# Performance work log

Hardware: AMD Instinct MI355X
Metric: run time of the kernel (lower is better)

The kernel has to match this reference:

```python
import jax, jax.numpy as jnp
import numpy as np


def _prelu(x, a):
    return jnp.where(x >= 0, x, a * x)


def setup_inputs() -> dict:
    key = jax.random.key(0)
    ks = jax.random.split(key, 10)
    B, N, h_dim, H_dim, g_dim, Kc, n = 64, 4096, 256, 1024, 512, 32, 2048
    hs = jax.random.normal(ks[0], (B, N, h_dim), dtype=jnp.float32)
    cs_o = jax.random.randint(ks[1], (B, N), 0, Kc, dtype=jnp.int32)

    def lin(k, fi, fo):
        return jax.random.normal(k, (fi, fo), dtype=jnp.float32) / np.sqrt(fi).astype(np.float32)

    a = jnp.full((1,), 0.25, dtype=jnp.float32)  # torch PReLU default
    return {
        "hs": hs,
        "W1": lin(ks[2], h_dim, H_dim), "b1": jnp.zeros((H_dim,), jnp.float32), "a1": a,
        "W2": lin(ks[3], H_dim, H_dim), "b2": jnp.zeros((H_dim,), jnp.float32), "a2": a,
        "W3": lin(ks[4], H_dim, H_dim), "b3": jnp.zeros((H_dim,), jnp.float32), "a3": a,
        "W4": lin(ks[5], H_dim, H_dim), "b4": jnp.zeros((H_dim,), jnp.float32), "a4": a,
        "W5": lin(ks[6], H_dim, H_dim), "b5": jnp.zeros((H_dim,), jnp.float32), "a5": a,
        "W6": lin(ks[7], H_dim, g_dim), "b6": jnp.zeros((g_dim,), jnp.float32),
        "cs_o": cs_o,
        "n": n,
    }


def reference(hs, W1, b1, a1, W2, b2, a2, W3, b3, a3, W4, b4, a4, W5, b5, a5, W6, b6, cs_o, n):
    B, N, h_dim = hs.shape
    cs = cs_o.at[:, n:].set(-1)                  # points >= n are unassigned
    K = int(jnp.max(cs)) + 1                      # static (concrete data)
    Ks = jnp.max(cs, axis=1)                      # [B] max cluster id per batch entry

    # per-cluster masked sums (vectorized segment-sum over all K at once)
    onehot = (cs[:, :, None] == jnp.arange(K)[None, None, :]).astype(hs.dtype)  # [B,N,K]
    Hk = jnp.einsum('bnk,bnh->bkh', onehot, hs)   # [B,K,h] sum of hs per cluster
    hn = hs[:, n, :]                              # [B,h] the point being assigned
    # H = [H_0..H_{K-1}, H_0+h_n..H_{K-1}+h_n, h_n]
    H = jnp.concatenate([Hk, Hk + hn[:, None, :], hn[:, None, :]], axis=1)  # [B,2K+1,h]

    mk = (jnp.sum(onehot, axis=1) > 0).astype(hs.dtype)  # [B,K] cluster non-empty
    gs_mask = jnp.concatenate([mk, mk, jnp.ones((B, 1), hs.dtype)], axis=1)[:, :, None]

    # 6-layer MLP g applied to all B*(2K+1) rows at once
    x = H.reshape(B * (2 * K + 1), h_dim)
    x = _prelu(x @ W1 + b1, a1)
    x = _prelu(x @ W2 + b2, a2)
    x = _prelu(x @ W3 + b3, a3)
    x = _prelu(x @ W4 + b4, a4)
    x = _prelu(x @ W5 + b5, a5)
    gs = (x @ W6 + b6).reshape(B, 2 * K + 1, -1) * gs_mask  # [B,2K+1,g]

    # G_k = sum_{j<K, j!=k} gs_j + gs_{k+K} ;  G_K = sum_{j<K} gs_j + gs_{2K}
    S = jnp.sum(gs[:, :K], axis=1)                                   # [B,g]
    G_head = (S[:, None, :] - gs[:, :K] + gs[:, K:2 * K]) * mk[:, :, None]
    G_last = S + gs[:, 2 * K]
    G = jnp.concatenate([G_head, G_last[:, None, :]], axis=1)        # [B,K+1,g]

    # per-batch correction: if Ks[b]==k (k<K-1), move G[b,-1] to slot k+1, zero last
    need = (Ks >= 0) & (Ks < K - 1)
    kidx = jnp.arange(K + 1)
    move = need[:, None] & (kidx[None, :] == (Ks + 1)[:, None])      # [B,K+1]
    G = jnp.where(move[:, :, None], G[:, K:K + 1, :], G)
    G = jnp.where((need[:, None] & (kidx[None, :] == K))[:, :, None], 0.0, G)
    G_mask = jnp.where(need[:, None] & (kidx[None, :] >= (Ks + 2)[:, None]),
                       0.0, jnp.ones((B, K + 1), hs.dtype))
    return (G, G_mask)
```

## Files before the change

### kernel.cpp

```cpp
#include <hip/hip_runtime.h>
#include <hip/hip_bf16.h>
#include <stdint.h>

using bf16x8 = __attribute__((ext_vector_type(8))) short;
using f32x4  = __attribute__((ext_vector_type(4))) float;

#define BATCH 64
#define NTOK  4096
#define HD    256
#define HDIM  1024
#define GD    512

__device__ __forceinline__ ushort f2bf(float f) {
  union { __hip_bfloat16 h; ushort u; } cv;
  cv.h = __float2bfloat16(f);
  return cv.u;
}

__device__ __forceinline__ void gload_lds16(const void* gsrc, void* ldst) {
  typedef const __attribute__((address_space(1))) uint32_t* gas_p;
  typedef __attribute__((address_space(3))) uint32_t* las_p;
  __builtin_amdgcn_global_load_lds((gas_p)(uintptr_t)gsrc, (las_p)(uintptr_t)ldst, 16, 0, 0);
}

struct WTArgs {
  const float* src[6];
  ushort* dst[6];
  int fi[6];
  int fo[6];
};

__global__ __launch_bounds__(256) void pre_kernel(WTArgs a,
                                                  const int* __restrict__ cs,
                                                  const int* __restrict__ nptr,
                                                  int* __restrict__ idx,
                                                  int* __restrict__ off,
                                                  int* __restrict__ cnt,
                                                  int* __restrict__ Ks,
                                                  int K) {
  __shared__ int csb[NTOK];
  __shared__ int hist[256 * 32];
  __shared__ int btot[32];
  __shared__ int bbase[32];
  __shared__ float tile[32][33];
  int t = threadIdx.x;
  if (blockIdx.x < BATCH) {
    int b = blockIdx.x;
    int n = *nptr;
    const int* csrow = cs + (size_t)b * NTOK;
    int mymax = -1;
    for (int i = t; i < n; i += 256) { int v = csrow[i]; csb[i] = v; mymax = max(mymax, v); }
#pragma unroll
    for (int k = 0; k < 32; ++k) hist[t * 32 + k] = 0;
    __syncthreads();
    int chunkN = (n + 255) >> 8;
    for (int c = 0; c < chunkN; ++c) {
      int i = c * 256 + t;
      if (i < n) hist[t * 32 + csb[i]]++;
    }
    __syncthreads();
    if (t < K) {
      int run = 0;
      for (int r = 0; r < 256; ++r) { int tmp = hist[r * 32 + t]; hist[r * 32 + t] = run; run += tmp; }
      btot[t] = run;
    }
    __syncthreads();
    if (t == 0) {
      int base = 0;
      for (int k = 0; k < K; ++k) { bbase[k] = base; base += btot[k]; }
    }
    __syncthreads();
    if (t < K) { off[b * K + t] = bbase[t]; cnt[b * K + t] = btot[t]; }
    int* idxb = idx + (size_t)b * NTOK;
    for (int c = 0; c < chunkN; ++c) {
      int i = c * 256 + t;
      if (i < n) {
        int k = csb[i];
        int s = bbase[k] + hist[t * 32 + k]++;
        idxb[s] = i;
      }
    }
    for (int o2 = 32; o2; o2 >>= 1) mymax = max(mymax, __shfl_down(mymax, o2));
    if ((t & 63) == 0) btot[16 + (t >> 6)] = mymax;
    __syncthreads();
    if (t == 0) {
      int r = btot[16];
      for (int i = 1; i < 4; ++i) r = max(r, btot[16 + i]);
      Ks[b] = r;
    }
  } else {
    int f = blockIdx.x - BATCH;
    int z = 0;
    while (true) {
      int nb = (a.fo[z] >> 5) * (a.fi[z] >> 5);
      if (f < nb) break;
      f -= nb; ++z;
    }
    int ncx = a.fo[z] >> 5;
    int cx = f % ncx, cy = f / ncx;
    int c0 = cx * 32, r0 = cy * 32;
    int fo = a.fo[z], fi = a.fi[z];
    const float* W = a.src[z];
    ushort* Wt = a.dst[z];
    int tx = t & 31, ty = t >> 5;
#pragma unroll
    for (int j = 0; j < 4; ++j)
      tile[ty + j * 8][tx] = W[(size_t)(r0 + ty + j * 8) * fo + (c0 + tx)];
    __syncthreads();
#pragma unroll
    for (int j = 0; j < 4; ++j)
      Wt[(size_t)(c0 + ty + j * 8) * fi + (r0 + tx)] = f2bf(tile[tx][ty + j * 8]);
  }
}

__global__ __launch_bounds__(256) void aggregate2_kernel(const float* __restrict__ hs,
                                                         const int* __restrict__ idx,
                                                         const int* __restrict__ off,
                                                         const int* __restrict__ cnt,
                                                         const int* __restrict__ nptr,
                                                         ushort* __restrict__ X,
                                                         int K, int M, int Mpad) {
  int b = blockIdx.x / K, k = blockIdx.x % K;
  int t = threadIdx.x;
  int g = t >> 6, l = t & 63;
  int n = *nptr;
  int c = cnt[b * K + k];
  int o = off[b * K + k];
  const float* hsb = hs + (size_t)b * NTOK * HD;
  const int* ids = idx + (size_t)b * NTOK + o;
  __shared__ int sid[256];
  __shared__ float part[4][HD];
  float ax = 0.f, ay = 0.f, az = 0.f, aw = 0.f;
  float bx = 0.f, by = 0.f, bz = 0.f, bw = 0.f;
  for (int j0 = 0; j0 < c; j0 += 256) {
    __syncthreads();
    if (j0 + t < c) sid[t] = ids[j0 + t];
    __syncthreads();
    int lim = min(256, c - j0);
    int j = g;
    for (; j + 4 < lim; j += 8) {
      float4 v0 = ((const float4*)&hsb[(size_t)sid[j] * HD])[l];
      float4 v1 = ((const float4*)&hsb[(size_t)sid[j + 4] * HD])[l];
      ax += v0.x; ay += v0.y; az += v0.z; aw += v0.w;
      bx += v1.x; by += v1.y; bz += v1.z; bw += v1.w;
    }
    for (; j < lim; j += 4) {
      float4 v = ((const float4*)&hsb[(size_t)sid[j] * HD])[l];
      ax += v.x; ay += v.y; az += v.z; aw += v.w;
    }
  }
  part[g][l * 4 + 0] = ax + bx;
  part[g][l * 4 + 1] = ay + by;
  part[g][l * 4 + 2] = az + bz;
  part[g][l * 4 + 3] = aw + bw;
  __syncthreads();
  float sum = ((part[0][t] + part[1][t]) + (part[2][t] + part[3][t]));
  float hn = hsb[(size_t)n * HD + t];
  int R = 2 * K + 1;
  X[((size_t)b * R + k) * HD + t]     = f2bf(sum);
  X[((size_t)b * R + K + k) * HD + t] = f2bf(sum + hn);
  if (k == 0) {
    X[((size_t)b * R + 2 * K) * HD + t] = f2bf(hn);
    for (int r = M + b; r < Mpad; r += BATCH) X[(size_t)r * HD + t] = 0;
  }
}

template <bool LAST>
__global__ __launch_bounds__(256) void gemm_kernel(const ushort* __restrict__ A,
                                                   const ushort* __restrict__ Bt,
                                                   const float* __restrict__ bias,
                                                   const float* __restrict__ aptr,
                                                   void* __restrict__ Cout,
                                                   int N, int Kd) {
  __shared__ ushort As[3][2][128 * 32];
  __shared__ ushort Bs[3][2][64 * 32];
  int tid = threadIdx.x;
  int lane = tid & 63, w = tid >> 6;
  int wr = w >> 1, wc = w & 1;
  int fr = lane & 15, fq = lane >> 4;

  int nwg = gridDim.x;
  int flat = blockIdx.x;
  int q8 = nwg >> 3, r8 = nwg & 7;
  int xcd = flat & 7, loc = flat >> 3;
  int swz = (xcd < r8 ? xcd * (q8 + 1) : r8 * (q8 + 1) + (xcd - r8) * q8) + loc;
  int NC = N >> 6;
  int brow = swz / NC, bcol = swz % NC;

  size_t row0 = (size_t)brow * 128;
  size_t col0 = (size_t)bcol * 64;

  const ushort* Abase = A + row0 * (size_t)Kd;
  const ushort* Bbase = Bt + col0 * (size_t)Kd;

  f32x4 acc[4][2] = {};

  int qA0 = w * 64 + lane;
  int qA1 = 256 + w * 64 + lane;
  int rA0 = qA0 >> 2, kA0 = (qA0 & 3) * 8;
  int rA1 = qA1 >> 2, kA1 = (qA1 & 3) * 8;
  int rB = qA0 >> 2, kB = (qA0 & 3) * 8;

  auto stage = [&](int buf, int k0) {
#pragma unroll
    for (int h = 0; h < 2; ++h) {
      int kh = k0 + h * 32;
      gload_lds16(Abase + (size_t)rA0 * Kd + kh + kA0, &As[buf][h][(w)     * 512]);
      gload_lds16(Abase + (size_t)rA1 * Kd + kh + kA1, &As[buf][h][(4 + w) * 512]);
      gload_lds16(Bbase + (size_t)rB  * Kd + kh + kB,  &Bs[buf][h][(w)     * 512]);
    }
  };

  int nt = Kd >> 6;
  stage(0, 0);
  stage(1, 64);
  for (int t = 0; t < nt; ++t) {
    if (t + 1 < nt) asm volatile("s_waitcnt vmcnt(6)" ::: "memory");
    else            asm volatile("s_waitcnt vmcnt(0)" ::: "memory");
    __builtin_amdgcn_s_barrier();
    __builtin_amdgcn_sched_barrier(0);
    int cur = t % 3;
    bf16x8 af[2][4], bfv[2][2];
#pragma unroll
    for (int h = 0; h < 2; ++h) {
#pragma unroll
      for (int m = 0; m < 4; ++m)
        af[h][m] = *(const bf16x8*)&As[cur][h][(wr * 64 + m * 16 + fr) * 32 + fq * 8];
#pragma unroll
      for (int nn = 0; nn < 2; ++nn)
        bfv[h][nn] = *(const bf16x8*)&Bs[cur][h][(wc * 32 + nn * 16 + fr) * 32 + fq * 8];
    }
    __builtin_amdgcn_s_setprio(1);
#pragma unroll
    for (int h = 0; h < 2; ++h)
#pragma unroll
      for (int m = 0; m < 4; ++m)
#pragma unroll
        for (int nn = 0; nn < 2; ++nn)
          acc[m][nn] = __builtin_amdgcn_mfma_f32_16x16x32_bf16(af[h][m], bfv[h][nn], acc[m][nn], 0, 0, 0);
    __builtin_amdgcn_s_setprio(0);
    if (t + 2 < nt) stage((t + 2) % 3, (t + 2) * 64);
  }

  float alpha = 0.f;
  if (!LAST) alpha = aptr[0];
#pragma unroll
  for (int nn = 0; nn < 2; ++nn) {
    size_t col = col0 + wc * 32 + nn * 16 + fr;
    float bv = bias[col];
#pragma unroll
    for (int m = 0; m < 4; ++m) {
      size_t rbase = row0 + wr * 64 + m * 16 + fq * 4;
#pragma unroll
      for (int j = 0; j < 4; ++j) {
        float v = acc[m][nn][j] + bv;
        if (!LAST) {
          v = (v >= 0.f) ? v : alpha * v;
          ((ushort*)Cout)[(rbase + j) * N + col] = f2bf(v);
        } else {
          ((float*)Cout)[(rbase + j) * N + col] = v;
        }
      }
    }
  }
}

__global__ __launch_bounds__(256) void final_kernel(const float* __restrict__ gs,
                                                    const int* __restrict__ counts,
                                                    const int* __restrict__ Ks,
                                                    float* __restrict__ out,
                                                    int K) {
  int b = blockIdx.x, t = threadIdx.x;
  __shared__ float mk[64];
  __shared__ int sks;
  if (t < K) mk[t] = (counts[b * K + t] > 0) ? 1.f : 0.f;
  if (t == 0) sks = Ks[b];
  __syncthreads();
  int ks = sks;
  bool need = (ks >= 0) && (ks < K - 1);
  const float* g = gs + (size_t)b * (2 * K + 1) * GD;
  float S0 = 0.f, S1 = 0.f;
  for (int k = 0; k < K; ++k) {
    S0 += g[(size_t)k * GD + t] * mk[k];
    S1 += g[(size_t)k * GD + t + 256] * mk[k];
  }
  float gl0 = S0 + g[(size_t)(2 * K) * GD + t];
  float gl1 = S1 + g[(size_t)(2 * K) * GD + t + 256];
  float* G  = out + (size_t)b * (K + 1) * GD;
  float* Gm = out + (size_t)BATCH * (K + 1) * GD + (size_t)b * (K + 1);
  for (int kk = 0; kk <= K; ++kk) {
    float v0, v1;
    if (kk == K)                  { v0 = need ? 0.f : gl0; v1 = need ? 0.f : gl1; }
    else if (need && kk == ks + 1){ v0 = gl0;              v1 = gl1; }
    else {
      v0 = mk[kk] * (S0 - g[(size_t)kk * GD + t]       + g[(size_t)(K + kk) * GD + t]);
      v1 = mk[kk] * (S1 - g[(size_t)kk * GD + t + 256] + g[(size_t)(K + kk) * GD + t + 256]);
    }
    G[(size_t)kk * GD + t]       = v0;
    G[(size_t)kk * GD + t + 256] = v1;
  }
  if (t <= K) Gm[t] = (need && t >= ks + 2) ? 0.f : 1.f;
}

extern "C" void kernel_launch(void* const* d_in, const int* in_sizes, int n_in,
                              void* d_out, int out_size, void* d_ws, size_t ws_size,
                              hipStream_t stream) {
  const float* hs = (const float*)d_in[0];
  const float* W[6]  = {(const float*)d_in[1], (const float*)d_in[4], (const float*)d_in[7],
                        (const float*)d_in[10], (const float*)d_in[13], (const float*)d_in[16]};
  const float* bb[6] = {(const float*)d_in[2], (const float*)d_in[5], (const float*)d_in[8],
                        (const float*)d_in[11], (const float*)d_in[14], (const float*)d_in[17]};
  const float* aa[5] = {(const float*)d_in[3], (const float*)d_in[6], (const float*)d_in[9],
                        (const float*)d_in[12], (const float*)d_in[15]};
  const int* cs   = (const int*)d_in[18];
  const int* nptr = (const int*)d_in[19];
  float* out = (float*)d_out;

  int K = out_size / (BATCH * (GD + 1)) - 1;
  int M = BATCH * (2 * K + 1);
  int Mpad = (M + 127) / 128 * 128;

  char* base = (char*)d_ws;
  size_t off_b = 0;
  auto alloc = [&](size_t bytes) {
    char* p = base + off_b;
    off_b = (off_b + bytes + 255) & ~(size_t)255;
    return p;
  };
  ushort* W1t  = (ushort*)alloc((size_t)HDIM * HD * 2);
  ushort* W2t  = (ushort*)alloc((size_t)HDIM * HDIM * 2);
  ushort* W3t  = (ushort*)alloc((size_t)HDIM * HDIM * 2);
  ushort* W4t  = (ushort*)alloc((size_t)HDIM * HDIM * 2);
  ushort* W5bt = (ushort*)alloc((size_t)HDIM * HDIM * 2);
  ushort* W6t  = (ushort*)alloc((size_t)GD * HDIM * 2);
  int* idx     = (int*)alloc((size_t)BATCH * NTOK * 4);
  int* offb    = (int*)alloc((size_t)BATCH * K * 4);
  int* cntb    = (int*)alloc((size_t)BATCH * K * 4);
  int* Ksb     = (int*)alloc(BATCH * 4);
  ushort* X    = (ushort*)alloc((size_t)Mpad * HD * 2);
  ushort* Y0   = (ushort*)alloc((size_t)Mpad * HDIM * 2);
  ushort* Y1   = (ushort*)alloc((size_t)Mpad * HDIM * 2);
  float*  gsb  = (float*)alloc((size_t)Mpad * GD * 4);
  (void)ws_size; (void)n_in; (void)in_sizes;

  WTArgs wa;
  wa.src[0] = W[0]; wa.dst[0] = W1t;  wa.fi[0] = HD;   wa.fo[0] = HDIM;
  wa.src[1] = W[1]; wa.dst[1] = W2t;  wa.fi[1] = HDIM; wa.fo[1] = HDIM;
  wa.src[2] = W[2]; wa.dst[2] = W3t;  wa.fi[2] = HDIM; wa.fo[2] = HDIM;
  wa.src[3] = W[3]; wa.dst[3] = W4t;  wa.fi[3] = HDIM; wa.fo[3] = HDIM;
  wa.src[4] = W[4]; wa.dst[4] = W5bt; wa.fi[4] = HDIM; wa.fo[4] = HDIM;
  wa.src[5] = W[5]; wa.dst[5] = W6t;  wa.fi[5] = HDIM; wa.fo[5] = GD;
  int nbw = 0;
  for (int z = 0; z < 6; ++z) nbw += (wa.fo[z] / 32) * (wa.fi[z] / 32);
  hipLaunchKernelGGL(pre_kernel, dim3(BATCH + nbw), dim3(256), 0, stream,
                     wa, cs, nptr, idx, offb, cntb, Ksb, K);

  hipLaunchKernelGGL(aggregate2_kernel, dim3(BATCH * K), dim3(256), 0, stream,
                     hs, idx, offb, cntb, nptr, X, K, M, Mpad);

  dim3 blk(256);
  int NR = Mpad / 128;
  hipLaunchKernelGGL((gemm_kernel<false>), dim3(NR * (HDIM / 64)), blk, 0, stream, X,   W1t,  bb[0], aa[0], (void*)Y0, HDIM, HD);
  hipLaunchKernelGGL((gemm_kernel<false>), dim3(NR * (HDIM / 64)), blk, 0, stream, Y0,  W2t,  bb[1], aa[1], (void*)Y1, HDIM, HDIM);
  hipLaunchKernelGGL((gemm_kernel<false>), dim3(NR * (HDIM / 64)), blk, 0, stream, Y1,  W3t,  bb[2], aa[2], (void*)Y0, HDIM, HDIM);
  hipLaunchKernelGGL((gemm_kernel<false>), dim3(NR * (HDIM / 64)), blk, 0, stream, Y0,  W4t,  bb[3], aa[3], (void*)Y1, HDIM, HDIM);
  hipLaunchKernelGGL((gemm_kernel<false>), dim3(NR * (HDIM / 64)), blk, 0, stream, Y1,  W5bt, bb[4], aa[4], (void*)Y0, HDIM, HDIM);
  hipLaunchKernelGGL((gemm_kernel<true>),  dim3(NR * (GD / 64)),   blk, 0, stream, Y0,  W6t,  bb[5], nullptr, (void*)gsb, GD, HDIM);

  hipLaunchKernelGGL(final_kernel, dim3(BATCH), dim3(256), 0, stream, gsb, cntb, Ksb, out, K);
}
```

Baseline: 166.8 us.

## Switch GEMM to two-stage double buffering and shrink pre-kernel histogram to ushort

The GEMM main loop moves from a three-buffer LDS pipeline, with manual vmcnt waits and priority hints, to a simpler two-buffer scheme. It issues the next tile's load at the top of each iteration and ends with a full __syncthreads. Less LDS per block plus launch_bounds(256,3) aims for more resident workgroups, at the cost of a shallower prefetch and a full barrier each iteration. The pre-kernel histogram changes from int to ushort to cut its LDS footprint, and the max reduction gets its own small shared array.

After: 148.5 us. -10.9%, faster.

```diff
diff --git a/kernel.cpp b/kernel.cpp
--- a/kernel.cpp
+++ b/kernel.cpp
@@ -39,9 +39,10 @@
                                                   int* __restrict__ Ks,
                                                   int K) {
   __shared__ int csb[NTOK];
-  __shared__ int hist[256 * 32];
+  __shared__ ushort hist[256 * 32];
   __shared__ int btot[32];
   __shared__ int bbase[32];
+  __shared__ int red[4];
   __shared__ float tile[32][33];
   int t = threadIdx.x;
   if (blockIdx.x < BATCH) {
@@ -61,7 +62,11 @@
     __syncthreads();
     if (t < K) {
       int run = 0;
-      for (int r = 0; r < 256; ++r) { int tmp = hist[r * 32 + t]; hist[r * 32 + t] = run; run += tmp; }
+      for (int r = 0; r < 256; ++r) {
+        int tmp = hist[r * 32 + t];
+        hist[r * 32 + t] = (ushort)run;
+        run += tmp;
+      }
       btot[t] = run;
     }
     __syncthreads();
@@ -76,16 +81,16 @@
       int i = c * 256 + t;
       if (i < n) {
         int k = csb[i];
-        int s = bbase[k] + hist[t * 32 + k]++;
+        int s = bbase[k] + (int)(hist[t * 32 + k]++);
         idxb[s] = i;
       }
     }
     for (int o2 = 32; o2; o2 >>= 1) mymax = max(mymax, __shfl_down(mymax, o2));
-    if ((t & 63) == 0) btot[16 + (t >> 6)] = mymax;
+    if ((t & 63) == 0) red[t >> 6] = mymax;
     __syncthreads();
     if (t == 0) {
-      int r = btot[16];
-      for (int i = 1; i < 4; ++i) r = max(r, btot[16 + i]);
+      int r = red[0];
+      for (int i = 1; i < 4; ++i) r = max(r, red[i]);
       Ks[b] = r;
     }
   } else {
@@ -166,14 +171,14 @@
 }
 
 template <bool LAST>
-__global__ __launch_bounds__(256) void gemm_kernel(const ushort* __restrict__ A,
-                                                   const ushort* __restrict__ Bt,
-                                                   const float* __restrict__ bias,
-                                                   const float* __restrict__ aptr,
-                                                   void* __restrict__ Cout,
-                                                   int N, int Kd) {
-  __shared__ ushort As[3][2][128 * 32];
-  __shared__ ushort Bs[3][2][64 * 32];
+__global__ __launch_bounds__(256, 3) void gemm_kernel(const ushort* __restrict__ A,
+                                                      const ushort* __restrict__ Bt,
+                                                      const float* __restrict__ bias,
+                                                      const float* __restrict__ aptr,
+                                                      void* __restrict__ Cout,
+                                                      int N, int Kd) {
+  __shared__ ushort As[2][2][128 * 32];
+  __shared__ ushort Bs[2][2][64 * 32];
   int tid = threadIdx.x;
   int lane = tid & 63, w = tid >> 6;
   int wr = w >> 1, wc = w & 1;
@@ -212,14 +217,11 @@
   };
 
   int nt = Kd >> 6;
+  int cur = 0;
   stage(0, 0);
-  stage(1, 64);
+  __syncthreads();
   for (int t = 0; t < nt; ++t) {
-    if (t + 1 < nt) asm volatile("s_waitcnt vmcnt(6)" ::: "memory");
-    else            asm volatile("s_waitcnt vmcnt(0)" ::: "memory");
-    __builtin_amdgcn_s_barrier();
-    __builtin_amdgcn_sched_barrier(0);
-    int cur = t % 3;
+    if (t + 1 < nt) stage(cur ^ 1, (t + 1) * 64);
     bf16x8 af[2][4], bfv[2][2];
 #pragma unroll
     for (int h = 0; h < 2; ++h) {
@@ -230,7 +232,6 @@
       for (int nn = 0; nn < 2; ++nn)
         bfv[h][nn] = *(const bf16x8*)&Bs[cur][h][(wc * 32 + nn * 16 + fr) * 32 + fq * 8];
     }
-    __builtin_amdgcn_s_setprio(1);
 #pragma unroll
     for (int h = 0; h < 2; ++h)
 #pragma unroll
@@ -238,8 +239,8 @@
 #pragma unroll
         for (int nn = 0; nn < 2; ++nn)
           acc[m][nn] = __builtin_amdgcn_mfma_f32_16x16x32_bf16(af[h][m], bfv[h][nn], acc[m][nn], 0, 0, 0);
-    __builtin_amdgcn_s_setprio(0);
-    if (t + 2 < nt) stage((t + 2) % 3, (t + 2) * 64);
+    __syncthreads();
+    cur ^= 1;
   }
 
   float alpha = 0.f;
```
